# Optimization experiments

Hardware: AMD Instinct MI355X
Metric: run time of the kernel (lower is better)

The kernel has to match this reference:

```python
import jax, jax.numpy as jnp
import numpy as np

ALPHA = 0.2  # LeakyReLU negative slope
NEG_BIG = -9e15


def setup_inputs() -> dict:
    key = jax.random.key(0)
    k1, k2, k3, k4 = jax.random.split(key, 4)
    B, N, F_in, F_out = 8, 2048, 256, 256
    x = jax.random.normal(k1, (B, N, F_in), dtype=jnp.float32)
    adj = jax.random.randint(k2, (B, N, N), 0, 2, dtype=jnp.int32)
    # Xavier-uniform init like nn.init.xavier_uniform_
    limW = float(np.sqrt(6.0 / (F_in + F_out)))
    W = jax.random.uniform(k3, (F_in, F_out), minval=-limW, maxval=limW, dtype=jnp.float32)
    lima = float(np.sqrt(6.0 / (2 * F_out + 1)))
    a = jax.random.uniform(k4, (2 * F_out, 1), minval=-lima, maxval=lima, dtype=jnp.float32)
    return {"x": x, "adj": adj, "W": W, "a": a}


def reference(x, adj, W, a):
    # x: (B,N,Fin), adj: (B,N,N), W: (Fin,Fout), a: (2*Fout,1)
    F_out = W.shape[1]
    Wh = jnp.einsum('bnf,fo->bno', x, W)            # (B,N,Fout)
    a1, a2 = a[:F_out, 0], a[F_out:, 0]
    # e[b,i,j] = leakyrelu(Wh[b,i]@a1 + Wh[b,j]@a2)  (equivalent to concat+matmul)
    e = (Wh @ a1)[:, :, None] + (Wh @ a2)[:, None, :]  # (B,N,N)
    e = jnp.where(e > 0, e, ALPHA * e)
    attention = jnp.where(adj > 0, e, NEG_BIG)
    attention = jax.nn.softmax(attention, axis=-1)
    # dropout is identity in eval mode (training=False)
    h_prime = jnp.einsum('bij,bjo->bio', attention, Wh)  # (B,N,Fout)
    return jax.nn.elu(h_prime)  # concat=True -> ELU
```

## Files before the change

### kernel.cpp

```cpp
#include <hip/hip_runtime.h>
#include <hip/hip_fp16.h>

typedef _Float16 f16;
typedef _Float16 half4 __attribute__((ext_vector_type(4)));
typedef _Float16 half8 __attribute__((ext_vector_type(8)));
typedef float f32x4 __attribute__((ext_vector_type(4)));

#define BATCH 8
#define NTOK 2048
#define FIN 256
#define FOUT 256
#define ALPHA 0.2f


__device__ __forceinline__ void gload16(const void* g, void* l) {
    __builtin_amdgcn_global_load_lds(
        (const __attribute__((address_space(1))) unsigned int*)(g),
        (__attribute__((address_space(3))) unsigned int*)(l), 16, 0, 0);
}

__global__ void k_wt(const float* __restrict__ W, f16* __restrict__ WT) {
    __shared__ float t[32][33];
    int o0 = blockIdx.x * 32, k0 = blockIdx.y * 32;
    int tx = threadIdx.x, ty = threadIdx.y;
    t[ty][tx] = W[(k0 + ty) * FOUT + o0 + tx];
    __syncthreads();
    WT[(o0 + ty) * FIN + (k0 + tx)] = (f16)t[tx][ty];
}

__global__ __launch_bounds__(256) void k_gp(const float* __restrict__ x,
                                            const f16* __restrict__ WT,
                                            const float* __restrict__ a,
                                            const int* __restrict__ adj,
                                            f16* __restrict__ WhT,
                                            float* __restrict__ s1,
                                            float* __restrict__ s2,
                                            unsigned long long* __restrict__ mask) {
    __shared__ __align__(16) char gsmem[46080];
    int t = threadIdx.x;
    int lane = t & 63, w = t >> 6;

    if (blockIdx.x >= 256) {
        int wid = (blockIdx.x - 256) * 4 + w;
        const int* base0 = adj + (size_t)wid * 8192;
        unsigned long long* mdst = mask + (size_t)wid * 128;
        for (int it = 0; it < 8; it++) {
            const int* base = base0 + it * 1024;
            int v[16];
#pragma unroll
            for (int k = 0; k < 16; k++) v[k] = base[k * 64 + lane];
            unsigned long long mv[16];
#pragma unroll
            for (int k = 0; k < 16; k++) mv[k] = __ballot(v[k] > 0);
            if (lane < 16) {
                unsigned long long r = mv[0];
#pragma unroll
                for (int k = 1; k < 16; k++) r = (lane == k) ? mv[k] : r;
                mdst[it * 16 + lane] = r;
            }
        }
        return;
    }

    f16* Ah = (f16*)gsmem;
    f16* Bt = (f16*)(gsmem + 9216);
    int m0 = blockIdx.x * 64;
    int lr = lane & 15, lg = lane >> 4;
    f32x4 acc[4][4] = {};

    for (int k0 = 0; k0 < FIN; k0 += 64) {
        {
            int r = t >> 2, c = (t & 3) * 16;
            const float* src = x + (size_t)(m0 + r) * FIN + k0 + c;
            f32x4 v0 = *(const f32x4*)(src);
            f32x4 v1 = *(const f32x4*)(src + 4);
            f32x4 v2 = *(const f32x4*)(src + 8);
            f32x4 v3 = *(const f32x4*)(src + 12);
            half8 h0, h1;
#pragma unroll
            for (int q = 0; q < 4; q++) {
                h0[q] = (f16)v0[q]; h0[q + 4] = (f16)v1[q];
                h1[q] = (f16)v2[q]; h1[q + 4] = (f16)v3[q];
            }
            f16* dst = Ah + r * 72 + c;
            *(half8*)dst = h0;
            *(half8*)(dst + 8) = h1;
        }
        {
            const f16* src = WT + (size_t)t * FIN + k0;
            f16* dst = Bt + t * 72;
#pragma unroll
            for (int q = 0; q < 8; q++)
                *(half8*)(dst + q * 8) = *(const half8*)(src + q * 8);
        }
        __syncthreads();
#pragma unroll
        for (int kc = 0; kc < 2; kc++) {
            int krow = kc * 32 + lg * 8;
            half8 af[4], bf[4];
#pragma unroll
            for (int fi = 0; fi < 4; fi++)
                af[fi] = *(half8*)(Ah + (fi * 16 + lr) * 72 + krow);
#pragma unroll
            for (int fo = 0; fo < 4; fo++)
                bf[fo] = *(half8*)(Bt + (w * 64 + fo * 16 + lr) * 72 + krow);
#pragma unroll
            for (int fi = 0; fi < 4; fi++)
#pragma unroll
                for (int fo = 0; fo < 4; fo++)
                    acc[fi][fo] = __builtin_amdgcn_mfma_f32_16x16x32_f16(
                        af[fi], bf[fo], acc[fi][fo], 0, 0, 0);
        }
        __syncthreads();
    }

    int b = m0 >> 11;
    int slab_i = (m0 & (NTOK - 1)) >> 6;
    int nbase = m0 & (NTOK - 1);

    float* sred = (float*)gsmem;
    f16* slab = (f16*)(gsmem + 9216);
    float a1v[4], a2v[4];
#pragma unroll
    for (int fo = 0; fo < 4; fo++) {
        int o = w * 64 + fo * 16 + lr;
        a1v[fo] = a[o];
        a2v[fo] = a[FOUT + o];
    }
#pragma unroll
    for (int fi = 0; fi < 4; fi++) {
        f32x4 p1 = {}, p2 = {};
#pragma unroll
        for (int fo = 0; fo < 4; fo++) {
            p1 += acc[fi][fo] * a1v[fo];
            p2 += acc[fi][fo] * a2v[fo];
        }
#pragma unroll
        for (int q = 0; q < 4; q++) {
#pragma unroll
            for (int d = 1; d < 16; d <<= 1) {
                p1[q] += __shfl_xor(p1[q], d);
                p2[q] += __shfl_xor(p2[q], d);
            }
        }
        if (lr == 0) {
            int row = fi * 16 + lg * 4;
#pragma unroll
            for (int q = 0; q < 4; q++) {
                sred[w * 64 + row + q] = p1[q];
                sred[256 + w * 64 + row + q] = p2[q];
            }
        }
    }
#pragma unroll
    for (int fi = 0; fi < 4; fi++) {
        int jg8 = fi * 2 + (lg >> 1), jq0 = (lg & 1) * 4;
#pragma unroll
        for (int fo = 0; fo < 4; fo++) {
            int o = w * 64 + fo * 16 + lr;
            half4 hv;
#pragma unroll
            for (int q = 0; q < 4; q++) hv[q] = (f16)acc[fi][fo][q];
            *(half4*)(slab + o * 64 + ((jg8 ^ (o & 7)) * 8) + jq0) = hv;
        }
    }
    __syncthreads();

    if (t < 64) {
        s1[(size_t)b * NTOK + nbase + t] =
            sred[t] + sred[64 + t] + sred[128 + t] + sred[192 + t];
    } else if (t < 128) {
        int r2 = t - 64;
        s2[(size_t)b * NTOK + nbase + r2] =
            sred[256 + r2] + sred[320 + r2] + sred[384 + r2] + sred[448 + r2];
    }
    {
        const int4* sl = (const int4*)slab;
        int4* gd = (int4*)(WhT + ((size_t)(b * 32 + slab_i) * 256) * 64);
#pragma unroll
        for (int i = 0; i < 8; i++) gd[i * 256 + t] = sl[i * 256 + t];
    }
}

__global__ __launch_bounds__(256) void k_rowmax(const float* __restrict__ s1,
                                                const float* __restrict__ s2,
                                                float* __restrict__ mrow) {
    __shared__ float red[4];
    int b = blockIdx.x, t = threadIdx.x;
    const float* s2b = s2 + (size_t)b * NTOK;
    float mx = -3.0e38f;
#pragma unroll
    for (int i = 0; i < 8; i++) mx = fmaxf(mx, s2b[t + i * 256]);
#pragma unroll
    for (int d = 1; d < 64; d <<= 1) mx = fmaxf(mx, __shfl_xor(mx, d));
    if ((t & 63) == 0) red[t >> 6] = mx;
    __syncthreads();
    float s2m = fmaxf(fmaxf(red[0], red[1]), fmaxf(red[2], red[3]));
#pragma unroll
    for (int i = 0; i < 8; i++) {
        int n = t + i * 256;
        float s = s1[(size_t)b * NTOK + n] + s2m;
        mrow[(size_t)b * NTOK + n] = fmaxf(s, ALPHA * s);
    }
}

__global__ __launch_bounds__(512, 2) void k_attn(const unsigned* __restrict__ mask32,
                                                 const f16* __restrict__ WhT,
                                                 const float* __restrict__ s1g,
                                                 const float* __restrict__ s2g,
                                                 const float* __restrict__ mg,
                                                 float* __restrict__ out) {
    __shared__ __align__(16) char smem[65536 + 8192 + 512];
    f16* Bl = (f16*)smem;
    float* s2_lds = (float*)(smem + 65536);
    float* lpart = (float*)(smem + 65536 + 8192);

    int b = blockIdx.x & 7;
    int i0 = (blockIdx.x >> 3) * 64;
    int t = threadIdx.x;
    int lane = t & 63, w = t >> 6;
    int js = w & 1, oh = (w >> 1) & 1, rg = w >> 2;
    int lr = lane & 15, lg = lane >> 4;

    ((f32x4*)s2_lds)[t] = ((const f32x4*)(s2g + (size_t)b * NTOK))[t];

    const char* wsrc = (const char*)WhT + (size_t)b * (32 * 32768);
    {
        const char* src = wsrc + (w * 4) * 1024 + lane * 16;
        char* dst = (char*)Bl + (w * 4) * 1024;
#pragma unroll
        for (int k = 0; k < 4; k++) gload16(src + k * 1024, dst + k * 1024);
    }

    int r0 = i0 + rg * 32 + lr, r1 = r0 + 16;
    float s1r0 = s1g[(size_t)b * NTOK + r0];
    float s1r1 = s1g[(size_t)b * NTOK + r1];
    float mx0 = mg[(size_t)b * NTOK + r0];
    float mx1 = mg[(size_t)b * NTOK + r1];
    const unsigned* mr0 = mask32 + (size_t)(b * NTOK + r0) * 64 + js;
    const unsigned* mr1 = mask32 + (size_t)(b * NTOK + r1) * 64 + js;

    f32x4 acc0[8] = {}, acc1[8] = {};
    float l0 = 0.f, l1 = 0.f;
    int rswz = ((js * 4 + lg) ^ (lr & 7)) * 8;

    unsigned bw0 = mr0[0], bw1 = mr1[0];

    __syncthreads();

    for (int s = 0; s < 32; s++) {
        int buf = s & 1;
        if (s < 31) {
            const char* src = wsrc + (size_t)(s + 1) * 32768 + (w * 4) * 1024 + lane * 16;
            char* dst = (char*)Bl + (buf ^ 1) * 32768 + (w * 4) * 1024;
#pragma unroll
            for (int k = 0; k < 4; k++) gload16(src + k * 1024, dst + k * 1024);
        }

        unsigned cw0 = bw0, cw1 = bw1;
        if (s < 31) { bw0 = mr0[(s + 1) * 2]; bw1 = mr1[(s + 1) * 2]; }
        unsigned bits0 = (cw0 >> (lg * 8)) & 0xffu;
        unsigned bits1 = (cw1 >> (lg * 8)) & 0xffu;

        int sb = s * 64 + js * 32 + lg * 8;
        f32x4 sA = *(const f32x4*)&s2_lds[sb];
        f32x4 sB = *(const f32x4*)&s2_lds[sb + 4];

        half8 ph0, ph1;
#pragma unroll
        for (int q = 0; q < 8; q++) {
            float sv = q < 4 ? sA[q & 3] : sB[q & 3];
            float sx = s1r0 + sv;
            float ev = fmaxf(sx, ALPHA * sx);
            float p = ((bits0 >> q) & 1) ? __expf(ev - mx0) : 0.f;
            l0 += p; ph0[q] = (f16)p;
            float sy = s1r1 + sv;
            float eu = fmaxf(sy, ALPHA * sy);
            float u = ((bits1 >> q) & 1) ? __expf(eu - mx1) : 0.f;
            l1 += u; ph1[q] = (f16)u;
        }

        const f16* bbase = Bl + buf * 16384 + (oh * 128 + lr) * 64 + rswz;
#pragma unroll
        for (int ot = 0; ot < 8; ot++) {
            half8 bf = *(const half8*)(bbase + ot * (16 * 64));
            acc0[ot] = __builtin_amdgcn_mfma_f32_16x16x32_f16(ph0, bf, acc0[ot], 0, 0, 0);
            acc1[ot] = __builtin_amdgcn_mfma_f32_16x16x32_f16(ph1, bf, acc1[ot], 0, 0, 0);
        }
        __syncthreads();
    }

    l0 += __shfl_xor(l0, 16); l0 += __shfl_xor(l0, 32);
    l1 += __shfl_xor(l1, 16); l1 += __shfl_xor(l1, 32);
    if (oh == 0 && lg == 0) {
        lpart[js * 64 + rg * 32 + lr] = l0;
        lpart[js * 64 + rg * 32 + 16 + lr] = l1;
    }
    __syncthreads();

    float* accx = (float*)smem;
    if (js == 1) {
#pragma unroll
        for (int ot = 0; ot < 8; ot++)
#pragma unroll
            for (int q = 0; q < 4; q++) {
                accx[(rg * 32 + lg * 4 + q) * 260 + oh * 128 + ot * 16 + lr] = acc0[ot][q];
                accx[(rg * 32 + 16 + lg * 4 + q) * 260 + oh * 128 + ot * 16 + lr] = acc1[ot][q];
            }
    }
    __syncthreads();
    if (js == 0) {
        f32x4 rl0, rl1;
#pragma unroll
        for (int q = 0; q < 4; q++) {
            int ra = rg * 32 + lg * 4 + q, rb = ra + 16;
            rl0[q] = 1.f / (lpart[ra] + lpart[64 + ra]);
            rl1[q] = 1.f / (lpart[rb] + lpart[64 + rb]);
        }
#pragma unroll
        for (int ot = 0; ot < 8; ot++) {
            int o = oh * 128 + ot * 16 + lr;
#pragma unroll
            for (int q = 0; q < 4; q++) {
                int ra = rg * 32 + lg * 4 + q;
                float u = (acc0[ot][q] + accx[ra * 260 + o]) * rl0[q];
                u = u > 0.f ? u : __expf(u) - 1.f;
                __builtin_nontemporal_store(u, &out[((size_t)(b * NTOK + i0 + ra)) * FOUT + o]);
                int rb = ra + 16;
                float v = (acc1[ot][q] + accx[rb * 260 + o]) * rl1[q];
                v = v > 0.f ? v : __expf(v) - 1.f;
                __builtin_nontemporal_store(v, &out[((size_t)(b * NTOK + i0 + rb)) * FOUT + o]);
            }
        }
    }
}

extern "C" void kernel_launch(void* const* d_in, const int* in_sizes, int n_in,
                              void* d_out, int out_size, void* d_ws, size_t ws_size,
                              hipStream_t stream) {
    const float* x = (const float*)d_in[0];
    const int* adj = (const int*)d_in[1];
    const float* W = (const float*)d_in[2];
    const float* a = (const float*)d_in[3];
    float* out = (float*)d_out;

    char* ws = (char*)d_ws;
    f16* WT = (f16*)ws;
    f16* WhT = (f16*)(ws + 131072);
    float* s1 = (float*)(ws + 131072 + 8388608);
    float* s2 = s1 + BATCH * NTOK;
    float* mrow = s2 + BATCH * NTOK;
    unsigned long long* mask64 =
        (unsigned long long*)(ws + 131072 + 8388608 + 196608);

    k_wt<<<dim3(FOUT / 32, FIN / 32), dim3(32, 32), 0, stream>>>(W, WT);
    k_gp<<<dim3(256 + 1024), 256, 0, stream>>>(x, WT, a, adj, WhT, s1, s2, mask64);
    k_rowmax<<<dim3(BATCH), 256, 0, stream>>>(s1, s2, mrow);
    k_attn<<<dim3(BATCH * NTOK / 64), 512, 0, stream>>>((const unsigned*)mask64, WhT,
                                                        s1, s2, mrow, out);
}
```

Measured before the change: 84.61 us.

## Fuse row-max into attention kernel and split adjacency packing from GEMM

Removes the separate single-wave-per-batch row-max kernel. Each attention block now recomputes the per-batch max of s2 from the s2 values it already loads into LDS, then derives the row softmax bound locally. The combined GEMM+mask-pack kernel is also split into two launches (GEMM first, then pack). This drops one tiny, poorly parallel launch and its global round trip. In exchange it adds one more launch for the split, and the pack work no longer overlaps the GEMM blocks within a single grid.

```diff
diff --git a/kernel.cpp b/kernel.cpp
--- a/kernel.cpp
+++ b/kernel.cpp
@@ -28,40 +28,39 @@
     WT[(o0 + ty) * FIN + (k0 + tx)] = (f16)t[tx][ty];
 }
 
-__global__ __launch_bounds__(256) void k_gp(const float* __restrict__ x,
-                                            const f16* __restrict__ WT,
-                                            const float* __restrict__ a,
-                                            const int* __restrict__ adj,
-                                            f16* __restrict__ WhT,
-                                            float* __restrict__ s1,
-                                            float* __restrict__ s2,
-                                            unsigned long long* __restrict__ mask) {
+__global__ __launch_bounds__(256) void k_pack(const int* __restrict__ adj,
+                                              unsigned long long* __restrict__ mask) {
+    int t = threadIdx.x;
+    int lane = t & 63, w = t >> 6;
+    int wid = blockIdx.x * 4 + w;
+    const int* base0 = adj + (size_t)wid * 8192;
+    unsigned long long* mdst = mask + (size_t)wid * 128;
+    for (int it = 0; it < 8; it++) {
+        const int* base = base0 + it * 1024;
+        int v[16];
+#pragma unroll
+        for (int k = 0; k < 16; k++) v[k] = base[k * 64 + lane];
+        unsigned long long mv[16];
+#pragma unroll
+        for (int k = 0; k < 16; k++) mv[k] = __ballot(v[k] > 0);
+        if (lane < 16) {
+            unsigned long long r = mv[0];
+#pragma unroll
+            for (int k = 1; k < 16; k++) r = (lane == k) ? mv[k] : r;
+            mdst[it * 16 + lane] = r;
+        }
+    }
+}
+
+__global__ __launch_bounds__(256) void k_gemm(const float* __restrict__ x,
+                                              const f16* __restrict__ WT,
+                                              const float* __restrict__ a,
+                                              f16* __restrict__ WhT,
+                                              float* __restrict__ s1,
+                                              float* __restrict__ s2) {
     __shared__ __align__(16) char gsmem[46080];
     int t = threadIdx.x;
     int lane = t & 63, w = t >> 6;
-
-    if (blockIdx.x >= 256) {
-        int wid = (blockIdx.x - 256) * 4 + w;
-        const int* base0 = adj + (size_t)wid * 8192;
-        unsigned long long* mdst = mask + (size_t)wid * 128;
-        for (int it = 0; it < 8; it++) {
-            const int* base = base0 + it * 1024;
-            int v[16];
-#pragma unroll
-            for (int k = 0; k < 16; k++) v[k] = base[k * 64 + lane];
-            unsigned long long mv[16];
-#pragma unroll
-            for (int k = 0; k < 16; k++) mv[k] = __ballot(v[k] > 0);
-            if (lane < 16) {
-                unsigned long long r = mv[0];
-#pragma unroll
-                for (int k = 1; k < 16; k++) r = (lane == k) ? mv[k] : r;
-                mdst[it * 16 + lane] = r;
-            }
-        }
-        return;
-    }
-
     f16* Ah = (f16*)gsmem;
     f16* Bt = (f16*)(gsmem + 9216);
     int m0 = blockIdx.x * 64;
@@ -182,38 +181,16 @@
     }
 }
 
-__global__ __launch_bounds__(256) void k_rowmax(const float* __restrict__ s1,
-                                                const float* __restrict__ s2,
-                                                float* __restrict__ mrow) {
-    __shared__ float red[4];
-    int b = blockIdx.x, t = threadIdx.x;
-    const float* s2b = s2 + (size_t)b * NTOK;
-    float mx = -3.0e38f;
-#pragma unroll
-    for (int i = 0; i < 8; i++) mx = fmaxf(mx, s2b[t + i * 256]);
-#pragma unroll
-    for (int d = 1; d < 64; d <<= 1) mx = fmaxf(mx, __shfl_xor(mx, d));
-    if ((t & 63) == 0) red[t >> 6] = mx;
-    __syncthreads();
-    float s2m = fmaxf(fmaxf(red[0], red[1]), fmaxf(red[2], red[3]));
-#pragma unroll
-    for (int i = 0; i < 8; i++) {
-        int n = t + i * 256;
-        float s = s1[(size_t)b * NTOK + n] + s2m;
-        mrow[(size_t)b * NTOK + n] = fmaxf(s, ALPHA * s);
-    }
-}
-
 __global__ __launch_bounds__(512, 2) void k_attn(const unsigned* __restrict__ mask32,
                                                  const f16* __restrict__ WhT,
                                                  const float* __restrict__ s1g,
                                                  const float* __restrict__ s2g,
-                                                 const float* __restrict__ mg,
                                                  float* __restrict__ out) {
-    __shared__ __align__(16) char smem[65536 + 8192 + 512];
+    __shared__ __align__(16) char smem[65536 + 8192 + 512 + 64];
     f16* Bl = (f16*)smem;
     float* s2_lds = (float*)(smem + 65536);
     float* lpart = (float*)(smem + 65536 + 8192);
+    float* wmax = (float*)(smem + 65536 + 8192 + 512);
 
     int b = blockIdx.x & 7;
     int i0 = (blockIdx.x >> 3) * 64;
@@ -222,7 +199,14 @@
     int js = w & 1, oh = (w >> 1) & 1, rg = w >> 2;
     int lr = lane & 15, lg = lane >> 4;
 
-    ((f32x4*)s2_lds)[t] = ((const f32x4*)(s2g + (size_t)b * NTOK))[t];
+    {
+        f32x4 sv4 = ((const f32x4*)(s2g + (size_t)b * NTOK))[t];
+        ((f32x4*)s2_lds)[t] = sv4;
+        float tmx = fmaxf(fmaxf(sv4[0], sv4[1]), fmaxf(sv4[2], sv4[3]));
+#pragma unroll
+        for (int d = 1; d < 64; d <<= 1) tmx = fmaxf(tmx, __shfl_xor(tmx, d));
+        if (lane == 0) wmax[w] = tmx;
+    }
 
     const char* wsrc = (const char*)WhT + (size_t)b * (32 * 32768);
     {
@@ -235,8 +219,6 @@
     int r0 = i0 + rg * 32 + lr, r1 = r0 + 16;
     float s1r0 = s1g[(size_t)b * NTOK + r0];
     float s1r1 = s1g[(size_t)b * NTOK + r1];
-    float mx0 = mg[(size_t)b * NTOK + r0];
-    float mx1 = mg[(size_t)b * NTOK + r1];
     const unsigned* mr0 = mask32 + (size_t)(b * NTOK + r0) * 64 + js;
     const unsigned* mr1 = mask32 + (size_t)(b * NTOK + r1) * 64 + js;
 
@@ -247,6 +229,14 @@
     unsigned bw0 = mr0[0], bw1 = mr1[0];
 
     __syncthreads();
+
+    float s2m = wmax[0];
+#pragma unroll
+    for (int k = 1; k < 8; k++) s2m = fmaxf(s2m, wmax[k]);
+    float tx0 = s1r0 + s2m;
+    float mx0 = fmaxf(tx0, ALPHA * tx0);
+    float tx1 = s1r1 + s2m;
+    float mx1 = fmaxf(tx1, ALPHA * tx1);
 
     for (int s = 0; s < 32; s++) {
         int buf = s & 1;
@@ -349,13 +339,12 @@
     f16* WhT = (f16*)(ws + 131072);
     float* s1 = (float*)(ws + 131072 + 8388608);
     float* s2 = s1 + BATCH * NTOK;
-    float* mrow = s2 + BATCH * NTOK;
     unsigned long long* mask64 =
         (unsigned long long*)(ws + 131072 + 8388608 + 196608);
 
     k_wt<<<dim3(FOUT / 32, FIN / 32), dim3(32, 32), 0, stream>>>(W, WT);
-    k_gp<<<dim3(256 + 1024), 256, 0, stream>>>(x, WT, a, adj, WhT, s1, s2, mask64);
-    k_rowmax<<<dim3(BATCH), 256, 0, stream>>>(s1, s2, mrow);
+    k_gemm<<<dim3(BATCH * NTOK / 64), 256, 0, stream>>>(x, WT, a, WhT, s1, s2);
+    k_pack<<<dim3(1024), 256, 0, stream>>>(adj, mask64);
     k_attn<<<dim3(BATCH * NTOK / 64), 512, 0, stream>>>((const unsigned*)mask64, WhT,
-                                                        s1, s2, mrow, out);
-}
+                                                        s1, s2, out);
+}
```

Result: slower. 91.19 us (+7.8%).
